# Optimization experiments

Measured on AMD Instinct MI355X. Metric: run time of the kernel, lower is better.

The kernel has to match this reference:

```python
import jax, jax.numpy as jnp
import numpy as np


def setup_inputs() -> dict:
    key = jax.random.key(0)
    k1, k2, k3 = jax.random.split(key, 3)
    B, N, D = 16, 2048, 128
    q = jax.random.normal(k1, (B, N, D), dtype=jnp.float32)
    k = jax.random.normal(k2, (B, D, N), dtype=jnp.float32)
    v = jax.random.normal(k3, (B, N, D), dtype=jnp.float32)
    return {"q": q, "k": k, "v": v}


def reference(q, k, v):
    # scores: [B, N, N] — note NO 1/sqrt(d) scaling, matching the source
    scores = jnp.einsum('bnd,bdm->bnm', q, k)
    probs = jax.nn.softmax(scores, axis=-1)
    out = jnp.einsum('bnm,bmd->bnd', probs, v)  # [B, N, D]
    return out
```

## Files before the change

### kernel.cpp

```cpp
#include <hip/hip_runtime.h>


typedef __attribute__((ext_vector_type(8))) _Float16 f16x8;
typedef __attribute__((ext_vector_type(16))) float f32x16;

constexpr int Bz = 16;
constexpr int Nn = 2048;
constexpr int Dd = 128;
constexpr int BM = 128;
constexpr int BN = 32;
constexpr int ITG = (Nn / 2) / BN;

__device__ __forceinline__ int swz(int r) { return (r ^ (r >> 3)) & 7; }
__device__ __forceinline__ int sw4(int d) { return ((d >> 1) ^ (d >> 3)) & 3; }

__device__ __forceinline__ uint pkrtz(float a, float b) {
    return __builtin_bit_cast(uint, __builtin_amdgcn_cvt_pkrtz(a, b));
}

__device__ __forceinline__ float exp2i(float x) {
    return __builtin_amdgcn_exp2f(x);
}

__global__ __launch_bounds__(512, 2)
void fattn_kernel(const float* __restrict__ qg,
                  const float* __restrict__ kg,
                  const float* __restrict__ vg,
                  float* __restrict__ og)
{
    __shared__ ushort lds_k[2][2][BN * Dd];
    __shared__ ushort lds_v[2][2][Dd * BN];
    __shared__ float  mlx[4][2][32];

    const int bid  = blockIdx.x;
    const int xcd  = bid & 7;
    const int idx  = bid >> 3;
    const int b    = xcd * 2 + (idx >> 4);
    const int q0   = (idx & 15) * BM;
    const int tid  = threadIdx.x;
    const int wv   = tid >> 6;
    const int lane = tid & 63;
    const int h    = lane >> 5;
    const int l31  = lane & 31;
    const int grp  = wv >> 2;
    const int wq   = wv & 3;
    const int n_base = grp * (Nn / 2);

    const int gtid = wq * 64 + lane;
    const int kgrp = gtid & 3;
    const int krow = gtid >> 2;
    const int vgrp = gtid & 15;
    const int vrow = gtid >> 4;
    const float* kbase = kg + (size_t)b * Dd * Nn;
    const float* vbase = vg + (size_t)b * Nn * Dd;
    float4 kr[4], vr[4];

    auto issue_loads = [&](int n0) {
        const int d0 = krow * 2;
        const float* s0 = kbase + (size_t)d0 * Nn + n0 + kgrp * 8;
        kr[0] = ((const float4*)s0)[0];
        kr[1] = ((const float4*)s0)[1];
        kr[2] = ((const float4*)(s0 + Nn))[0];
        kr[3] = ((const float4*)(s0 + Nn))[1];
        const int kk0 = vrow * 2;
        const float* t0 = vbase + (size_t)(n0 + kk0) * Dd + vgrp * 8;
        vr[0] = ((const float4*)t0)[0];
        vr[1] = ((const float4*)t0)[1];
        vr[2] = ((const float4*)(t0 + Dd))[0];
        vr[3] = ((const float4*)(t0 + Dd))[1];
    };
    auto write_lds = [&](int buf) {
        uint* kw = (uint*)lds_k[grp][buf];
        const float* av = (const float*)&kr[0];
        const float* bv = (const float*)&kr[2];
        #pragma unroll
        for (int j = 0; j < 8; ++j) {
            const int n = kgrp * 8 + j;
            kw[n * (Dd / 2) + (krow ^ (swz(n) << 2))] = pkrtz(av[j], bv[j]);
        }
        uint* vw = (uint*)lds_v[grp][buf];
        const float* cv = (const float*)&vr[0];
        const float* dv = (const float*)&vr[2];
        #pragma unroll
        for (int j = 0; j < 8; ++j) {
            const int dd = vgrp * 8 + j;
            vw[dd * (BN / 2) + (vrow ^ (sw4(dd) << 2))] = pkrtz(cv[j], dv[j]);
        }
    };

    f16x8 qf[8];
    {
        const float* qp = qg + (size_t)(b * Nn + q0 + wq * 32 + l31) * Dd + h * 8;
        #pragma unroll
        for (int c = 0; c < 8; ++c) {
            float4 x0 = *(const float4*)(qp + c * 16);
            float4 x1 = *(const float4*)(qp + c * 16 + 4);
            const float xv[8] = {x0.x, x0.y, x0.z, x0.w, x1.x, x1.y, x1.z, x1.w};
            union { f16x8 v; _Float16 e[8]; } u;
            #pragma unroll
            for (int j = 0; j < 8; ++j)
                u.e[j] = (_Float16)(xv[j] * 1.44269504088896340736f);
            qf[c] = u.v;
        }
    }
    f32x16 accO[4];
    #pragma unroll
    for (int dt = 0; dt < 4; ++dt)
        #pragma unroll
        for (int r = 0; r < 16; ++r) accO[dt][r] = 0.f;
    float m_i = -1e30f, l_i = 0.f;

    auto consume = [&](const ushort* kb, const ushort* vb) {
        f32x16 accS;
        #pragma unroll
        for (int r = 0; r < 16; ++r) accS[r] = 0.f;
        {
            const int sw = swz(l31) << 3;
            __builtin_amdgcn_s_setprio(1);
            #pragma unroll
            for (int c = 0; c < 8; ++c) {
                f16x8 kf = *(const f16x8*)&kb[l31 * Dd + ((c * 16 + h * 8) ^ sw)];
                accS = __builtin_amdgcn_mfma_f32_32x32x16_f16(kf, qf[c], accS, 0, 0, 0);
            }
            __builtin_amdgcn_s_setprio(0);
        }

        float t0 = fmaxf(accS[0], accS[1]),  t1 = fmaxf(accS[2], accS[3]);
        float t2 = fmaxf(accS[4], accS[5]),  t3 = fmaxf(accS[6], accS[7]);
        float t4 = fmaxf(accS[8], accS[9]),  t5 = fmaxf(accS[10], accS[11]);
        float t6 = fmaxf(accS[12], accS[13]), t7 = fmaxf(accS[14], accS[15]);
        float u0 = fmaxf(t0, t1), u1 = fmaxf(t2, t3);
        float u2 = fmaxf(t4, t5), u3 = fmaxf(t6, t7);
        float mx = fmaxf(fmaxf(u0, u1), fmaxf(u2, u3));
        mx = fmaxf(mx, __shfl_xor(mx, 32, 64));

        if (!__all(mx <= m_i + 8.f)) {
            const float mn = fmaxf(m_i, mx);
            const float al = exp2i(m_i - mn);
            m_i = mn;
            l_i *= al;
            #pragma unroll
            for (int dt = 0; dt < 4; ++dt)
                #pragma unroll
                for (int r = 0; r < 16; ++r) accO[dt][r] *= al;
        }
        float local = 0.f;
        #pragma unroll
        for (int r = 0; r < 16; ++r) {
            const float p = exp2i(accS[r] - m_i);
            accS[r] = p;
            local += p;
        }
        l_i += local;

        f16x8 vf[4][2];
        #pragma unroll
        for (int dt = 0; dt < 4; ++dt) {
            const int drow = dt * 32 + l31;
            const int sv = sw4(drow) << 3;
            vf[dt][0] = *(const f16x8*)&vb[drow * BN + ((8 * h) ^ sv)];
            vf[dt][1] = *(const f16x8*)&vb[drow * BN + ((16 + 8 * h) ^ sv)];
        }

        const uint pA0 = pkrtz(accS[0],  accS[1]);
        const uint pA1 = pkrtz(accS[2],  accS[3]);
        const uint pB0 = pkrtz(accS[4],  accS[5]);
        const uint pB1 = pkrtz(accS[6],  accS[7]);
        const uint pC0 = pkrtz(accS[8],  accS[9]);
        const uint pC1 = pkrtz(accS[10], accS[11]);
        const uint pD0 = pkrtz(accS[12], accS[13]);
        const uint pD1 = pkrtz(accS[14], accS[15]);
        const uint yA0 = __shfl_xor(pA0, 32, 64);
        const uint yA1 = __shfl_xor(pA1, 32, 64);
        const uint yB0 = __shfl_xor(pB0, 32, 64);
        const uint yB1 = __shfl_xor(pB1, 32, 64);
        const uint yC0 = __shfl_xor(pC0, 32, 64);
        const uint yC1 = __shfl_xor(pC1, 32, 64);
        const uint yD0 = __shfl_xor(pD0, 32, 64);
        const uint yD1 = __shfl_xor(pD1, 32, 64);
        union { uint u[4]; f16x8 v; } P0, P1;
        P0.u[0] = h ? yB0 : pA0;
        P0.u[1] = h ? yB1 : pA1;
        P0.u[2] = h ? pB0 : yA0;
        P0.u[3] = h ? pB1 : yA1;
        P1.u[0] = h ? yD0 : pC0;
        P1.u[1] = h ? yD1 : pC1;
        P1.u[2] = h ? pD0 : yC0;
        P1.u[3] = h ? pD1 : yC1;
        const f16x8 pf0 = P0.v, pf1 = P1.v;

        __builtin_amdgcn_s_setprio(1);
        #pragma unroll
        for (int dt = 0; dt < 4; ++dt) {
            accO[dt] = __builtin_amdgcn_mfma_f32_32x32x16_f16(vf[dt][0], pf0, accO[dt], 0, 0, 0);
            accO[dt] = __builtin_amdgcn_mfma_f32_32x32x16_f16(vf[dt][1], pf1, accO[dt], 0, 0, 0);
        }
        __builtin_amdgcn_s_setprio(0);
    };

    issue_loads(n_base);
    write_lds(0);
    issue_loads(n_base + BN);
    __syncthreads();

    for (int it = 0; it < ITG; it += 2) {
        write_lds(1);
        if (it + 2 < ITG) issue_loads(n_base + (it + 2) * BN);
        consume(lds_k[grp][0], lds_v[grp][0]);
        __syncthreads();
        if (it + 2 < ITG) write_lds(0);
        if (it + 3 < ITG) issue_loads(n_base + (it + 3) * BN);
        consume(lds_k[grp][1], lds_v[grp][1]);
        __syncthreads();
    }

    float l_full = l_i + __shfl_xor(l_i, 32, 64);
    const int pair = wq;
    if (grp == 1 && h == 0) {
        mlx[pair][0][l31] = m_i;
        mlx[pair][1][l31] = l_full;
    }
    float* sc = (float*)lds_k;

    #pragma unroll
    for (int rnd = 0; rnd < 2; ++rnd) {
        if (grp == 1 && (pair >> 1) == rnd) {
            float* base = sc + (pair & 1) * 4096 + lane * 64;
            #pragma unroll
            for (int dt = 0; dt < 4; ++dt)
                #pragma unroll
                for (int r = 0; r < 16; ++r)
                    base[(dt * 16 + r) ^ l31] = accO[dt][r];
        }
        __syncthreads();
        if (grp == 0 && (pair >> 1) == rnd) {
            const float m_B = mlx[pair][0][l31];
            const float l_B = mlx[pair][1][l31];
            const float ms  = fmaxf(m_i, m_B);
            const float aA  = exp2i(m_i - ms);
            const float aB  = exp2i(m_B - ms);
            const float inv = 1.f / (aA * l_full + aB * l_B);
            const float* base = sc + (pair & 1) * 4096 + lane * 64;
            float* ob = og + (size_t)(b * Nn + q0 + wq * 32 + l31) * Dd;
            #pragma unroll
            for (int dt = 0; dt < 4; ++dt) {
                #pragma unroll
                for (int g = 0; g < 4; ++g) {
                    float4 val;
                    #pragma unroll
                    for (int j = 0; j < 4; ++j) {
                        const int r = 4 * g + j;
                        const float o = aA * accO[dt][r] + aB * base[(dt * 16 + r) ^ l31];
                        ((float*)&val)[j] = o * inv;
                    }
                    *(float4*)(ob + dt * 32 + 8 * g + 4 * h) = val;
                }
            }
        }
        __syncthreads();
    }
}

extern "C" void kernel_launch(void* const* d_in, const int* in_sizes, int n_in,
                              void* d_out, int out_size, void* d_ws, size_t ws_size,
                              hipStream_t stream) {
    const float* q = (const float*)d_in[0];
    const float* k = (const float*)d_in[1];
    const float* v = (const float*)d_in[2];
    float* o = (float*)d_out;
    (void)d_ws; (void)ws_size; (void)in_sizes; (void)n_in; (void)out_size;
    fattn_kernel<<<dim3(Bz * (Nn / BM)), dim3(512), 0, stream>>>(q, k, v, o);
}
```

Baseline: 136.3 us.

## Pre-pack K/V into swizzled fp16 tile images and DMA them directly into LDS

Adds a prepass kernel that converts K and V to fp16 and lays them out as per-tile swizzled images in the workspace, in exactly the LDS layout the attention kernel expects. The attention kernel then fills LDS with global_load_lds direct copies instead of loading fp32 into registers, converting and scattering to LDS. This halves the bytes the main kernel reads for K/V and removes the register staging and conversion work, at the cost of an extra launch and a full extra pass over K and V each call. The loop becomes single-tile double buffered, and the V fragment loads move ahead of the softmax.

```diff
diff --git a/kernel.cpp b/kernel.cpp
--- a/kernel.cpp
+++ b/kernel.cpp
@@ -9,7 +9,8 @@
 constexpr int Dd = 128;
 constexpr int BM = 128;
 constexpr int BN = 32;
-constexpr int ITG = (Nn / 2) / BN;
+constexpr int NT = Nn / BN;
+constexpr int ITG = NT / 2;
 
 __device__ __forceinline__ int swz(int r) { return (r ^ (r >> 3)) & 7; }
 __device__ __forceinline__ int sw4(int d) { return ((d >> 1) ^ (d >> 3)) & 3; }
@@ -22,10 +23,67 @@
     return __builtin_amdgcn_exp2f(x);
 }
 
+__global__ __launch_bounds__(256)
+void build_images(const float* __restrict__ kg, const float* __restrict__ vg,
+                  uint* __restrict__ kimg, uint* __restrict__ vimg)
+{
+    __shared__ float sk[32][129];
+    __shared__ float sv[32][129];
+    const int bid = blockIdx.x;
+    const int b   = bid >> 6;
+    const int tt  = bid & 63;
+    const int n0  = tt * 32;
+    const int t   = threadIdx.x;
+
+    const float* kb = kg + (size_t)b * Dd * Nn;
+    #pragma unroll
+    for (int i = 0; i < 16; ++i) {
+        const int d = i * 8 + (t >> 5);
+        const int n = t & 31;
+        sk[n][d] = kb[(size_t)d * Nn + n0 + n];
+    }
+    const float* vb = vg + (size_t)b * Nn * Dd;
+    #pragma unroll
+    for (int i = 0; i < 16; ++i) {
+        const int kk = i * 2 + (t >> 7);
+        const int d  = t & 127;
+        sv[kk][d] = vb[(size_t)(n0 + kk) * Dd + d];
+    }
+    __syncthreads();
+
+    uint2* ko = (uint2*)(kimg + (size_t)bid * 2048);
+    #pragma unroll
+    for (int j = 0; j < 4; ++j) {
+        const int I = t * 4 + j;
+        const int n = I >> 5, m = I & 31;
+        const int dq = m ^ ((swz(n) << 1) ^ (n & 8));
+        const int d0 = dq * 4;
+        uint2 pv;
+        pv.x = pkrtz(sk[n][d0],     sk[n][d0 + 1]);
+        pv.y = pkrtz(sk[n][d0 + 2], sk[n][d0 + 3]);
+        ko[I] = pv;
+    }
+    uint2* vo = (uint2*)(vimg + (size_t)bid * 2048);
+    #pragma unroll
+    for (int j = 0; j < 4; ++j) {
+        const int I = t * 4 + j;
+        const int rowp = I >> 3, mm = I & 7;
+        const int d  = rowp ^ ((rowp >> 5) & 1);
+        const int kq = mm ^ (sw4(d) << 1);
+        const int k0 = kq * 4;
+        uint2 pv;
+        pv.x = pkrtz(sv[k0][d],     sv[k0 + 1][d]);
+        pv.y = pkrtz(sv[k0 + 2][d], sv[k0 + 3][d]);
+        vo[I] = pv;
+    }
+}
+
+typedef __attribute__((address_space(3))) uint lds_u32;
+
 __global__ __launch_bounds__(512, 2)
 void fattn_kernel(const float* __restrict__ qg,
-                  const float* __restrict__ kg,
-                  const float* __restrict__ vg,
+                  const uint* __restrict__ kimg,
+                  const uint* __restrict__ vimg,
                   float* __restrict__ og)
 {
     __shared__ ushort lds_k[2][2][BN * Dd];
@@ -44,47 +102,19 @@
     const int l31  = lane & 31;
     const int grp  = wv >> 2;
     const int wq   = wv & 3;
-    const int n_base = grp * (Nn / 2);
-
-    const int gtid = wq * 64 + lane;
-    const int kgrp = gtid & 3;
-    const int krow = gtid >> 2;
-    const int vgrp = gtid & 15;
-    const int vrow = gtid >> 4;
-    const float* kbase = kg + (size_t)b * Dd * Nn;
-    const float* vbase = vg + (size_t)b * Nn * Dd;
-    float4 kr[4], vr[4];
-
-    auto issue_loads = [&](int n0) {
-        const int d0 = krow * 2;
-        const float* s0 = kbase + (size_t)d0 * Nn + n0 + kgrp * 8;
-        kr[0] = ((const float4*)s0)[0];
-        kr[1] = ((const float4*)s0)[1];
-        kr[2] = ((const float4*)(s0 + Nn))[0];
-        kr[3] = ((const float4*)(s0 + Nn))[1];
-        const int kk0 = vrow * 2;
-        const float* t0 = vbase + (size_t)(n0 + kk0) * Dd + vgrp * 8;
-        vr[0] = ((const float4*)t0)[0];
-        vr[1] = ((const float4*)t0)[1];
-        vr[2] = ((const float4*)(t0 + Dd))[0];
-        vr[3] = ((const float4*)(t0 + Dd))[1];
-    };
-    auto write_lds = [&](int buf) {
-        uint* kw = (uint*)lds_k[grp][buf];
-        const float* av = (const float*)&kr[0];
-        const float* bv = (const float*)&kr[2];
-        #pragma unroll
-        for (int j = 0; j < 8; ++j) {
-            const int n = kgrp * 8 + j;
-            kw[n * (Dd / 2) + (krow ^ (swz(n) << 2))] = pkrtz(av[j], bv[j]);
-        }
-        uint* vw = (uint*)lds_v[grp][buf];
-        const float* cv = (const float*)&vr[0];
-        const float* dv = (const float*)&vr[2];
-        #pragma unroll
-        for (int j = 0; j < 8; ++j) {
-            const int dd = vgrp * 8 + j;
-            vw[dd * (BN / 2) + (vrow ^ (sw4(dd) << 2))] = pkrtz(cv[j], dv[j]);
+
+    auto dma_tile = [&](int timg, int buf) {
+        const uint* ksrc = kimg + (size_t)timg * 2048;
+        const uint* vsrc = vimg + (size_t)timg * 2048;
+        uint* kdst = (uint*)lds_k[grp][buf];
+        uint* vdst = (uint*)lds_v[grp][buf];
+        #pragma unroll
+        for (int r = 0; r < 2; ++r) {
+            const int off = (wq * 2 + r) * 256;
+            __builtin_amdgcn_global_load_lds(ksrc + off + lane * 4,
+                                             (lds_u32*)(kdst + off), 16, 0, 0);
+            __builtin_amdgcn_global_load_lds(vsrc + off + lane * 4,
+                                             (lds_u32*)(vdst + off), 16, 0, 0);
         }
     };
 
@@ -116,13 +146,24 @@
         for (int r = 0; r < 16; ++r) accS[r] = 0.f;
         {
             const int sw = swz(l31) << 3;
+            const int rx = (l31 & 8) << 2;
             __builtin_amdgcn_s_setprio(1);
             #pragma unroll
             for (int c = 0; c < 8; ++c) {
-                f16x8 kf = *(const f16x8*)&kb[l31 * Dd + ((c * 16 + h * 8) ^ sw)];
+                f16x8 kf = *(const f16x8*)&kb[l31 * Dd + ((c * 16 + h * 8) ^ sw ^ rx)];
                 accS = __builtin_amdgcn_mfma_f32_32x32x16_f16(kf, qf[c], accS, 0, 0, 0);
             }
             __builtin_amdgcn_s_setprio(0);
+        }
+
+        f16x8 vf[4][2];
+        #pragma unroll
+        for (int dt = 0; dt < 4; ++dt) {
+            const int drow = dt * 32 + l31;
+            const int rowp = drow ^ ((drow >> 5) & 1);
+            const int sv = sw4(drow) << 3;
+            vf[dt][0] = *(const f16x8*)&vb[rowp * BN + ((8 * h) ^ sv)];
+            vf[dt][1] = *(const f16x8*)&vb[rowp * BN + ((16 + 8 * h) ^ sv)];
         }
 
         float t0 = fmaxf(accS[0], accS[1]),  t1 = fmaxf(accS[2], accS[3]);
@@ -144,22 +185,15 @@
                 #pragma unroll
                 for (int r = 0; r < 16; ++r) accO[dt][r] *= al;
         }
-        float local = 0.f;
-        #pragma unroll
-        for (int r = 0; r < 16; ++r) {
-            const float p = exp2i(accS[r] - m_i);
-            accS[r] = p;
-            local += p;
-        }
-        l_i += local;
-
-        f16x8 vf[4][2];
-        #pragma unroll
-        for (int dt = 0; dt < 4; ++dt) {
-            const int drow = dt * 32 + l31;
-            const int sv = sw4(drow) << 3;
-            vf[dt][0] = *(const f16x8*)&vb[drow * BN + ((8 * h) ^ sv)];
-            vf[dt][1] = *(const f16x8*)&vb[drow * BN + ((16 + 8 * h) ^ sv)];
+        #pragma unroll
+        for (int r = 0; r < 16; ++r) accS[r] = exp2i(accS[r] - m_i);
+        {
+            float a0 = accS[0] + accS[1],   a1 = accS[2] + accS[3];
+            float a2 = accS[4] + accS[5],   a3 = accS[6] + accS[7];
+            float a4 = accS[8] + accS[9],   a5 = accS[10] + accS[11];
+            float a6 = accS[12] + accS[13], a7 = accS[14] + accS[15];
+            float b0 = a0 + a1, b1 = a2 + a3, b2 = a4 + a5, b3 = a6 + a7;
+            l_i += (b0 + b1) + (b2 + b3);
         }
 
         const uint pA0 = pkrtz(accS[0],  accS[1]);
@@ -198,19 +232,13 @@
         __builtin_amdgcn_s_setprio(0);
     };
 
-    issue_loads(n_base);
-    write_lds(0);
-    issue_loads(n_base + BN);
+    const int tbase = b * NT + grp * ITG;
+    dma_tile(tbase, 0);
     __syncthreads();
 
-    for (int it = 0; it < ITG; it += 2) {
-        write_lds(1);
-        if (it + 2 < ITG) issue_loads(n_base + (it + 2) * BN);
-        consume(lds_k[grp][0], lds_v[grp][0]);
-        __syncthreads();
-        if (it + 2 < ITG) write_lds(0);
-        if (it + 3 < ITG) issue_loads(n_base + (it + 3) * BN);
-        consume(lds_k[grp][1], lds_v[grp][1]);
+    for (int t = 0; t < ITG; ++t) {
+        if (t + 1 < ITG) dma_tile(tbase + t + 1, (t + 1) & 1);
+        consume(lds_k[grp][t & 1], lds_v[grp][t & 1]);
         __syncthreads();
     }
 
@@ -268,6 +296,9 @@
     const float* k = (const float*)d_in[1];
     const float* v = (const float*)d_in[2];
     float* o = (float*)d_out;
-    (void)d_ws; (void)ws_size; (void)in_sizes; (void)n_in; (void)out_size;
-    fattn_kernel<<<dim3(Bz * (Nn / BM)), dim3(512), 0, stream>>>(q, k, v, o);
-}
+    (void)in_sizes; (void)n_in; (void)out_size; (void)ws_size;
+    uint* kimg = (uint*)d_ws;
+    uint* vimg = kimg + (size_t)Bz * NT * 2048;
+    build_images<<<dim3(Bz * NT), dim3(256), 0, stream>>>(k, v, kimg, vimg);
+    fattn_kernel<<<dim3(Bz * (Nn / BM)), dim3(512), 0, stream>>>(q, kimg, vimg, o);
+}
```

Result: slower. 147.8 us (+8.4%).
